# Optimization experiments

Measured on AMD Instinct MI355X. Metric: run time of the kernel, lower is better.

## Reference

```python
import jax, jax.numpy as jnp
import numpy as np

EPS = 1e-5  # pyg LayerNorm default eps


def _graph_ln(x):
    # pyg.nn.norm.LayerNorm(affine=False), default mode='graph', batch=None:
    # normalizes over ALL elements of the tensor (x - x.mean()) / x.std(unbiased=False)
    m = x.mean()
    v = jnp.mean((x - m) ** 2)
    return (x - m) * jax.lax.rsqrt(v + EPS)


def _cheb_conv(x, row, col, w, W, b):
    # ChebConv, normalization='sym', lambda_max=2 => scaled Laplacian
    # L_hat = L - I = -D^{-1/2} A D^{-1/2} (self-loops removed, weighted)
    # x: [B,N,C_in], row/col: [E], w: [E], W: [K,C_in,C_out], b: [C_out]
    N = x.shape[1]
    w = jnp.where(row == col, 0.0, w)  # remove_self_loops
    deg = jnp.zeros((N,), x.dtype).at[row].add(w)
    dinv = jnp.where(deg > 0, jax.lax.rsqrt(jnp.maximum(deg, 1e-12)), 0.0)
    norm = -(dinv[row] * w * dinv[col])  # [E]

    def prop(t):  # out[i] += norm_e * t[j] for edge (j=row -> i=col)
        msg = norm[None, :, None] * t[:, row, :]  # [B,E,C]
        return jnp.zeros_like(t).at[:, col, :].add(msg)

    Tx0 = x
    out = jnp.einsum('bnc,cd->bnd', Tx0, W[0])
    Tx1 = prop(x)
    out = out + jnp.einsum('bnc,cd->bnd', Tx1, W[1])
    for k in range(2, W.shape[0]):
        Tx2 = 2.0 * prop(Tx1) - Tx0
        out = out + jnp.einsum('bnc,cd->bnd', Tx2, W[k])
        Tx0, Tx1 = Tx1, Tx2
    return out + b


def setup_inputs() -> dict:
    key = jax.random.key(0)
    ks = jax.random.split(key, 8)
    B, N, C, E, L, K = 8, 2048, 256, 32768, 3, 3
    node_feature = jax.random.normal(ks[0], (B, N, C), dtype=jnp.float32)
    edge_index = jax.random.randint(ks[1], (L, 2, E), 0, N)
    edge_weight = jax.random.uniform(ks[2], (L, E), dtype=jnp.float32)
    s = 1.0 / np.sqrt(C)
    cheb_w = jax.random.normal(ks[3], (L, K, C, C), dtype=jnp.float32) * s
    cheb_b = jnp.zeros((L, C), dtype=jnp.float32)
    mlp_w = jax.random.normal(ks[4], (L, C, C), dtype=jnp.float32) * s
    mlp_b = jax.random.normal(ks[5], (L, C), dtype=jnp.float32) * 0.01
    return {"node_feature": node_feature, "edge_weight": edge_weight,
            "cheb_w": cheb_w, "cheb_b": cheb_b, "mlp_w": mlp_w,
            "mlp_b": mlp_b, "edge_index": edge_index}


def reference(node_feature, edge_weight, cheb_w, cheb_b, mlp_w, mlp_b, edge_index):
    h = node_feature  # [B,N,C]
    L = cheb_w.shape[0]
    for l in range(L):
        h_res = h
        hn = _graph_ln(h)
        hc = _cheb_conv(hn, edge_index[l, 0], edge_index[l, 1],
                        edge_weight[l], cheb_w[l], cheb_b[l])
        h = hc + h_res
        h_res = h
        hn = _graph_ln(h)
        hm = jax.nn.gelu(jnp.einsum('bnc,cd->bnd', hn, mlp_w[l]) + mlp_b[l],
                         approximate=False)  # dropout is identity at inference
        h = hm + h_res
    return h.mean(axis=1)  # [B,C]
```

## Files before the change

kernel.cpp:

```cpp
#include <hip/hip_runtime.h>

#define BATCH   8
#define NNODE   2048
#define CH      256
#define NEDGE   32768
#define NLAYER  3
#define MROWS   (NNODE*BATCH)
#define KCAT    (3*CH)
#define NTOT    (MROWS*CH)

typedef _Float16 half8 __attribute__((ext_vector_type(8)));
typedef _Float16 half4 __attribute__((ext_vector_type(4)));
typedef float    f32x4 __attribute__((ext_vector_type(4)));

#define OFF_ACAT   ((size_t)0)
#define OFF_HF     ((size_t)25165824)
#define OFF_WT     ((size_t)33554432)
#define OFF_MT     ((size_t)34734080)
#define OFF_PARTA  ((size_t)35127296)
#define OFF_PARTB  ((size_t)35135488)
#define OFF_CS     ((size_t)35143680)
#define OFF_CSM    ((size_t)35152896)
#define OFF_DEG    ((size_t)35155968)
#define OFF_CNT    ((size_t)35180544)
#define OFF_ELIST  ((size_t)35205120)
#define OFF_R1     ((size_t)36777984)
#define OFF_R2     ((size_t)36802560)

__device__ __forceinline__ void async_lds16(const void* g, void* l) {
  __builtin_amdgcn_global_load_lds((const __attribute__((address_space(1))) void*)g,
                                   (__attribute__((address_space(3))) void*)l, 16, 0, 0);
}

__global__ __launch_bounds__(256) void k_init(const float* __restrict__ x,
                                              _Float16* __restrict__ Acat,
                                              float2* __restrict__ part,
                                              const float* __restrict__ cheb_w,
                                              const float* __restrict__ mlp_w,
                                              _Float16* __restrict__ Wt,
                                              _Float16* __restrict__ Mt,
                                              float* __restrict__ deg,
                                              unsigned int* __restrict__ count) {
  __shared__ float rs[512];
  __shared__ _Float16 lt[64][72];
  const int blk = blockIdx.x, t = threadIdx.x;
  if (blk < 1024) {
    int tid = blk*256 + t;
    float s = 0.f, s2 = 0.f;
    for (int i = tid; i < NTOT/4; i += 1024*256) {
      int c4 = i & 63, b = (i >> 6) & 7, n = i >> 9;
      float4 v = ((const float4*)x)[((b*NNODE + n) << 6) + c4];
      half4 o; o[0]=(_Float16)v.x; o[1]=(_Float16)v.y; o[2]=(_Float16)v.z; o[3]=(_Float16)v.w;
      *(half4*)&Acat[(size_t)(i >> 6)*KCAT + c4*4] = o;
      s  += v.x + v.y + v.z + v.w;
      s2 += v.x*v.x + v.y*v.y + v.z*v.z + v.w*v.w;
    }
    rs[t] = s; rs[256+t] = s2; __syncthreads();
    for (int o = 128; o > 0; o >>= 1) {
      if (t < o) { rs[t] += rs[t+o]; rs[256+t] += rs[256+t+o]; }
      __syncthreads();
    }
    if (t == 0) part[blk] = make_float2(rs[0], rs[256]);
  } else if (blk < 1048) {
    int i = (blk - 1024)*256 + t;
    if (i < NLAYER*NNODE) { deg[i] = 0.f; count[i] = 0u; }
  } else {
    const int tile = blk - 1048;
    const int rr = t >> 4, c4 = t & 15;
    if (tile < 144) {
      const int l = tile / 48, rem = tile % 48;
      const int kk = rem / 16, q = rem % 16, ci = q >> 2, ni = q & 3;
      const float4* W  = (const float4*)cheb_w + ((size_t)((l*3 + kk)*CH + ci*64))*64 + ni*16;
      const float4* W2 = (const float4*)cheb_w + ((size_t)((l*3 + 2 )*CH + ci*64))*64 + ni*16;
      #pragma unroll
      for (int p = 0; p < 4; ++p) {
        const int r = p*16 + rr;
        float4 v = W[(size_t)r*64 + c4];
        if (kk == 0) {
          float4 v2 = W2[(size_t)r*64 + c4];
          v.x -= v2.x; v.y -= v2.y; v.z -= v2.z; v.w -= v2.w;
        } else if (kk == 2) {
          v.x *= 2.f; v.y *= 2.f; v.z *= 2.f; v.w *= 2.f;
        }
        lt[c4*4+0][r] = (_Float16)v.x; lt[c4*4+1][r] = (_Float16)v.y;
        lt[c4*4+2][r] = (_Float16)v.z; lt[c4*4+3][r] = (_Float16)v.w;
      }
      __syncthreads();
      const int nr = t >> 2, ch2 = t & 3;
      #pragma unroll
      for (int pp = 0; pp < 2; ++pp) {
        const int ch = ch2 + pp*4;
        half8 v = *(const half8*)&lt[nr][ch*8];
        *(half8*)&Wt[((size_t)(l*CH + ni*64 + nr))*KCAT + kk*256 + ci*64 + ch*8] = v;
      }
    } else {
      const int m = tile - 144;
      const int l = m / 16, q = m % 16, ci = q >> 2, ni = q & 3;
      const float4* W = (const float4*)mlp_w + ((size_t)(l*CH + ci*64))*64 + ni*16;
      #pragma unroll
      for (int p = 0; p < 4; ++p) {
        const int r = p*16 + rr;
        float4 v = W[(size_t)r*64 + c4];
        lt[c4*4+0][r] = (_Float16)v.x; lt[c4*4+1][r] = (_Float16)v.y;
        lt[c4*4+2][r] = (_Float16)v.z; lt[c4*4+3][r] = (_Float16)v.w;
      }
      __syncthreads();
      const int nr = t >> 2, ch2 = t & 3;
      #pragma unroll
      for (int pp = 0; pp < 2; ++pp) {
        const int ch = ch2 + pp*4;
        half8 v = *(const half8*)&lt[nr][ch*8];
        *(half8*)&Mt[((size_t)(l*CH + ni*64 + nr))*CH + ci*64 + ch*8] = v;
      }
    }
  }
}

__global__ __launch_bounds__(256) void k_edge_scatter(const int* __restrict__ ei,
                                                      const float* __restrict__ ew,
                                                      float* deg, unsigned int* count,
                                                      unsigned int* elist,
                                                      const _Float16* __restrict__ Wt,
                                                      const _Float16* __restrict__ Mt,
                                                      float* __restrict__ cs,
                                                      float* __restrict__ csM,
                                                      float* __restrict__ out_zero) {
  const int blk = blockIdx.x, t = threadIdx.x;
  if (blk < 384) {
    int i = blk*256 + t;
    int l = i / NEDGE, e = i % NEDGE;
    const int* rows = ei + l*2*NEDGE;
    const int* cols = rows + NEDGE;
    int r = rows[e], c = cols[e];
    float w = (r == c) ? 0.f : ew[i];
    atomicAdd(&deg[l*NNODE + r], w);
    unsigned int slot = atomicAdd(&count[l*NNODE + c], 1u);
    if (slot < 64u) elist[(size_t)(l*NNODE + c)*64 + slot] = (unsigned int)e;
  } else if (blk < 393) {
    int idx = blk - 384, l = idx / 3, kk = idx % 3, n = t;
    const half8* row = (const half8*)&Wt[((size_t)(l*CH + n))*KCAT + kk*256];
    float s = 0.f;
    #pragma unroll 4
    for (int j = 0; j < 32; ++j) {
      half8 v = row[j];
      s += (float)v[0]+(float)v[1]+(float)v[2]+(float)v[3]
         + (float)v[4]+(float)v[5]+(float)v[6]+(float)v[7];
    }
    cs[(l*3 + kk)*CH + n] = s;
  } else if (blk < 396) {
    int l = blk - 393, n = t;
    const half8* row = (const half8*)&Mt[((size_t)(l*CH + n))*CH];
    float s = 0.f;
    #pragma unroll 4
    for (int j = 0; j < 32; ++j) {
      half8 v = row[j];
      s += (float)v[0]+(float)v[1]+(float)v[2]+(float)v[3]
         + (float)v[4]+(float)v[5]+(float)v[6]+(float)v[7];
    }
    csM[l*CH + n] = s;
  } else {
    for (int i = t; i < BATCH*CH; i += 256) out_zero[i] = 0.f;
  }
}

template<int SRC_OFF, int DST_OFF, int RMODE>
__global__ __launch_bounds__(256) void k_prop(_Float16* __restrict__ Acat,
                                              const int* __restrict__ rows,
                                              const float* __restrict__ ew_l,
                                              const float* __restrict__ deg_l,
                                              const unsigned int* __restrict__ count,
                                              const unsigned int* __restrict__ el,
                                              float* __restrict__ r1_l,
                                              float* __restrict__ r2_l) {
  const int blk = blockIdx.x, t = threadIdx.x;
  const int b = blk & 7, dgrp = blk >> 3;
  const int w = t >> 6, lane = t & 63;
  const int dst = dgrp*4 + w;
  unsigned int c = count[dst]; if (c > 64u) c = 64u;
  const float dc = deg_l[dst];
  const float ic = dc > 0.f ? rsqrtf(fmaxf(dc, 1e-12f)) : 0.f;
  int srcv = 0; float nmv = 0.f;
  if (lane < (int)c) {
    unsigned int e = el[(size_t)dst*64 + lane];
    srcv = rows[e];
    float wv = (srcv == dst) ? 0.f : ew_l[e];
    float dr = deg_l[srcv];
    float ir = dr > 0.f ? rsqrtf(fmaxf(dr, 1e-12f)) : 0.f;
    nmv = -(ir * wv * ic);
  }
  if (RMODE && b == 0) {
    float rv = nmv;
    if (RMODE == 2) rv = (lane < (int)c) ? nmv * r1_l[srcv] : 0.f;
    #pragma unroll
    for (int o = 32; o > 0; o >>= 1) rv += __shfl_xor(rv, o);
    if (lane == 0) { if (RMODE == 1) r1_l[dst] = rv; else r2_l[dst] = rv; }
  }
  float a0 = 0.f, a1 = 0.f, a2 = 0.f, a3 = 0.f;
  const _Float16* base = Acat + SRC_OFF + b*KCAT + lane*4;
  #define PROP_STEP(i)                                                            \
    {                                                                             \
      int   src = __builtin_amdgcn_readlane(srcv, (i));                           \
      int   nbi = __builtin_amdgcn_readlane(__builtin_bit_cast(int, nmv), (i));   \
      float nm  = __builtin_bit_cast(float, nbi);                                 \
      half4 v = *(const half4*)&base[(size_t)src*8*KCAT];                         \
      a0 += nm*(float)v[0]; a1 += nm*(float)v[1];                                 \
      a2 += nm*(float)v[2]; a3 += nm*(float)v[3];                                 \
    }
  unsigned int i = 0;
  for (; i + 4 <= c; i += 4) { PROP_STEP(i) PROP_STEP(i+1) PROP_STEP(i+2) PROP_STEP(i+3) }
  for (; i < c; ++i) { PROP_STEP(i) }
  #undef PROP_STEP
  half4 o; o[0] = (_Float16)a0; o[1] = (_Float16)a1; o[2] = (_Float16)a2; o[3] = (_Float16)a3;
  *(half4*)&Acat[(size_t)(dst*8 + b)*KCAT + DST_OFF + lane*4] = o;
}

template<int KSTEPS, int DO_GELU>
__global__ __launch_bounds__(256) void k_gemm(const _Float16* __restrict__ A, int lda,
                                              const _Float16* __restrict__ Bt, int ldb,
                                              const float* __restrict__ bias,
                                              const float* __restrict__ cs,
                                              const float* __restrict__ r1,
                                              const float* __restrict__ r2,
                                              const float2* __restrict__ part_in,
                                              float2* __restrict__ part_out,
                                              const _Float16* __restrict__ R, int ldr,
                                              _Float16* __restrict__ O, int ldo) {
  __shared__ _Float16 Als[64*64];
  __shared__ _Float16 Bls[64*64];
  __shared__ float red[512];
  __shared__ float mv[2];
  const int bm = blockIdx.x, bn = blockIdx.y;
  const int t = threadIdx.x;
  const int w = t >> 6, lane = t & 63;
  const int quad = lane >> 4, l16 = lane & 15;
  const int wm = w & 1, wn = w >> 1;

  {
    float s = 0.f, s2 = 0.f;
    for (int i = t; i < 1024; i += 256) { float2 p = part_in[i]; s += p.x; s2 += p.y; }
    red[t] = s; red[256+t] = s2; __syncthreads();
    for (int o = 128; o > 0; o >>= 1) {
      if (t < o) { red[t] += red[t+o]; red[256+t] += red[256+t+o]; }
      __syncthreads();
    }
    if (t == 0) {
      float mean = red[0] * (1.f/(float)NTOT);
      float var  = red[256] * (1.f/(float)NTOT) - mean*mean;
      mv[0] = mean; mv[1] = rsqrtf(var + 1e-5f);
    }
    __syncthreads();
  }
  const float mean = mv[0], istd = mv[1];

  f32x4 acc00 = {0.f,0.f,0.f,0.f};
  f32x4 acc01 = acc00, acc10 = acc00, acc11 = acc00;

  const int c0 = w*64 + lane, c1 = 256 + w*64 + lane;
  const int r0 = c0 >> 3, s0 = (c0 & 7) ^ (r0 & 7);
  const int r1i = c1 >> 3, s1 = (c1 & 7) ^ (r1i & 7);
  const _Float16* ga0 = A  + (size_t)(bm*64 + r0)*lda + s0*8;
  const _Float16* ga1 = A  + (size_t)(bm*64 + r1i)*lda + s1*8;
  const _Float16* gb0 = Bt + (size_t)(bn*64 + r0)*ldb + s0*8;
  const _Float16* gb1 = Bt + (size_t)(bn*64 + r1i)*ldb + s1*8;
  _Float16* lA0 = &Als[w*512];
  _Float16* lA1 = &Als[2048 + w*512];
  _Float16* lB0 = &Bls[w*512];
  _Float16* lB1 = &Bls[2048 + w*512];

  const int ra0 = wm*32 + l16, ra1 = ra0 + 16;
  const int rb0 = wn*32 + l16, rb1 = rb0 + 16;

  for (int ks = 0; ks < KSTEPS; ++ks) {
    async_lds16(ga0, lA0); async_lds16(ga1, lA1);
    async_lds16(gb0, lB0); async_lds16(gb1, lB1);
    ga0 += 64; ga1 += 64; gb0 += 64; gb1 += 64;
    __syncthreads();
    #pragma unroll
    for (int kh = 0; kh < 2; ++kh) {
      const int q = kh*4 + quad;
      half8 a0 = *(const half8*)&Als[ra0*64 + (q ^ (ra0 & 7))*8];
      half8 a1 = *(const half8*)&Als[ra1*64 + (q ^ (ra1 & 7))*8];
      half8 b0 = *(const half8*)&Bls[rb0*64 + (q ^ (rb0 & 7))*8];
      half8 b1 = *(const half8*)&Bls[rb1*64 + (q ^ (rb1 & 7))*8];
      acc00 = __builtin_amdgcn_mfma_f32_16x16x32_f16(a0, b0, acc00, 0, 0, 0);
      acc01 = __builtin_amdgcn_mfma_f32_16x16x32_f16(a0, b1, acc01, 0, 0, 0);
      acc10 = __builtin_amdgcn_mfma_f32_16x16x32_f16(a1, b0, acc10, 0, 0, 0);
      acc11 = __builtin_amdgcn_mfma_f32_16x16x32_f16(a1, b1, acc11, 0, 0, 0);
    }
    __syncthreads();
  }

  float s = 0.f, s2 = 0.f;
  const int gm0 = bm*64 + wm*32, gn0 = bn*64 + wn*32;
  const float mi = -mean * istd;
  #pragma unroll
  for (int i = 0; i < 2; ++i) {
    #pragma unroll
    for (int j = 0; j < 2; ++j) {
      f32x4 a = (i == 0) ? (j == 0 ? acc00 : acc01) : (j == 0 ? acc10 : acc11);
      const int col = gn0 + j*16 + l16;
      const float bv = bias[col];
      const float c0v = cs[col];
      float c1v = 0.f, c2v = 0.f;
      if (!DO_GELU) { c1v = cs[256 + col]; c2v = cs[512 + col]; }
      #pragma unroll
      for (int r = 0; r < 4; ++r) {
        const int row = gm0 + i*16 + quad*4 + r;
        float v;
        if (DO_GELU) {
          v = istd*a[r] + mi*c0v + bv;
          v = 0.5f*v*(1.f + erff(v*0.70710678118654752f));
        } else {
          const int node = row >> 3;
          v = istd*a[r] + mi*(c0v + r1[node]*c1v + r2[node]*c2v) + bv;
        }
        float hv = (float)R[(size_t)row*ldr + col] + v;
        O[(size_t)row*ldo + col] = (_Float16)hv;
        s += hv; s2 += hv*hv;
      }
    }
  }
  red[t] = s; red[256+t] = s2; __syncthreads();
  for (int o = 128; o > 0; o >>= 1) {
    if (t < o) { red[t] += red[t+o]; red[256+t] += red[256+t+o]; }
    __syncthreads();
  }
  if (t == 0) part_out[blockIdx.y*gridDim.x + blockIdx.x] = make_float2(red[0], red[256]);
}

__global__ __launch_bounds__(256) void k_mean(const _Float16* __restrict__ Acat,
                                              float* __restrict__ out) {
  int b = blockIdx.x & 7, chunk = blockIdx.x >> 3;
  int c = threadIdx.x;
  float s = 0.f;
  for (int k = 0; k < 256; ++k) {
    int n = chunk*256 + k;
    s += (float)Acat[(size_t)(n*8 + b)*KCAT + c];
  }
  atomicAdd(&out[(b << 8) + c], s * (1.f/(float)NNODE));
}

extern "C" void kernel_launch(void* const* d_in, const int* in_sizes, int n_in,
                              void* d_out, int out_size, void* d_ws, size_t ws_size,
                              hipStream_t stream) {
  const float* x      = (const float*)d_in[0];
  const float* ew     = (const float*)d_in[1];
  const float* cheb_w = (const float*)d_in[2];
  const float* cheb_b = (const float*)d_in[3];
  const float* mlp_w  = (const float*)d_in[4];
  const float* mlp_b  = (const float*)d_in[5];
  const int*   ei     = (const int*)d_in[6];
  float* out = (float*)d_out;

  char* ws = (char*)d_ws;
  _Float16*     Acat  = (_Float16*)(ws + OFF_ACAT);
  _Float16*     Hf    = (_Float16*)(ws + OFF_HF);
  _Float16*     Wt    = (_Float16*)(ws + OFF_WT);
  _Float16*     Mt    = (_Float16*)(ws + OFF_MT);
  float2*       partA = (float2*)(ws + OFF_PARTA);
  float2*       partB = (float2*)(ws + OFF_PARTB);
  float*        cs    = (float*)(ws + OFF_CS);
  float*        csM   = (float*)(ws + OFF_CSM);
  float*        deg   = (float*)(ws + OFF_DEG);
  unsigned int* cnt   = (unsigned int*)(ws + OFF_CNT);
  unsigned int* elist = (unsigned int*)(ws + OFF_ELIST);
  float*        r1    = (float*)(ws + OFF_R1);
  float*        r2    = (float*)(ws + OFF_R2);

  k_init<<<1240, 256, 0, stream>>>(x, Acat, partA, cheb_w, mlp_w, Wt, Mt, deg, cnt);
  k_edge_scatter<<<397, 256, 0, stream>>>(ei, ew, deg, cnt, elist, Wt, Mt, cs, csM, out);

  for (int l = 0; l < NLAYER; ++l) {
    const int* rows_l = ei + l*2*NEDGE;
    const float* ew_l = ew + l*NEDGE;
    const float* deg_l = deg + l*NNODE;
    const unsigned int* cnt_l = cnt + l*NNODE;
    const unsigned int* el_l  = elist + (size_t)l*NNODE*64;
    float* r1_l = r1 + l*NNODE;
    float* r2_l = r2 + l*NNODE;

    k_prop<0, 256, 1><<<4096, 256, 0, stream>>>(
        Acat, rows_l, ew_l, deg_l, cnt_l, el_l, r1_l, r2_l);
    k_prop<256, 512, 2><<<4096, 256, 0, stream>>>(
        Acat, rows_l, ew_l, deg_l, cnt_l, el_l, r1_l, r2_l);
    k_gemm<12, 0><<<dim3(256, 4), 256, 0, stream>>>(
        Acat, KCAT, Wt + (size_t)l*CH*KCAT, KCAT, cheb_b + l*CH,
        cs + l*3*CH, r1_l, r2_l, partA, partB,
        Acat, KCAT, Hf, CH);
    k_gemm<4, 1><<<dim3(256, 4), 256, 0, stream>>>(
        Hf, CH, Mt + (size_t)l*CH*CH, CH, mlp_b + l*CH,
        csM + l*CH, r1_l, r2_l, partB, partA,
        Hf, CH, Acat, KCAT);
  }

  k_mean<<<64, 256, 0, stream>>>(Acat, out);
}
```

Before: 287.6 us.

## Enlarge GEMM tile to 128x64, widen prop loads, halve partial-sum blocks

The GEMM kernels now compute a 128x64 output tile per block, with each wave holding 4x2 MFMA accumulators. This doubles A-tile LDS and the register footprint but reuses B fragments across more rows, and it halves the grid. The propagation kernel now has each wave cover two batches with 8-wide half loads per lane, halving its block count and widening the gather accesses. The init kernel's statistics partials are cut from 1024 to 512 blocks, and the GEMM reducers read only NPART entries.

Result: faster. 274.8 us (-4.5%).

```diff
diff --git a/kernel.cpp b/kernel.cpp
--- a/kernel.cpp
+++ b/kernel.cpp
@@ -27,6 +27,8 @@
 #define OFF_R1     ((size_t)36777984)
 #define OFF_R2     ((size_t)36802560)
 
+#define NPART 512
+
 __device__ __forceinline__ void async_lds16(const void* g, void* l) {
   __builtin_amdgcn_global_load_lds((const __attribute__((address_space(1))) void*)g,
                                    (__attribute__((address_space(3))) void*)l, 16, 0, 0);
@@ -44,10 +46,10 @@
   __shared__ float rs[512];
   __shared__ _Float16 lt[64][72];
   const int blk = blockIdx.x, t = threadIdx.x;
-  if (blk < 1024) {
+  if (blk < 512) {
     int tid = blk*256 + t;
     float s = 0.f, s2 = 0.f;
-    for (int i = tid; i < NTOT/4; i += 1024*256) {
+    for (int i = tid; i < NTOT/4; i += 512*256) {
       int c4 = i & 63, b = (i >> 6) & 7, n = i >> 9;
       float4 v = ((const float4*)x)[((b*NNODE + n) << 6) + c4];
       half4 o; o[0]=(_Float16)v.x; o[1]=(_Float16)v.y; o[2]=(_Float16)v.z; o[3]=(_Float16)v.w;
@@ -61,11 +63,11 @@
       __syncthreads();
     }
     if (t == 0) part[blk] = make_float2(rs[0], rs[256]);
-  } else if (blk < 1048) {
-    int i = (blk - 1024)*256 + t;
+  } else if (blk < 536) {
+    int i = (blk - 512)*256 + t;
     if (i < NLAYER*NNODE) { deg[i] = 0.f; count[i] = 0u; }
   } else {
-    const int tile = blk - 1048;
+    const int tile = blk - 536;
     const int rr = t >> 4, c4 = t & 15;
     if (tile < 144) {
       const int l = tile / 48, rem = tile % 48;
@@ -173,9 +175,10 @@
                                               float* __restrict__ r1_l,
                                               float* __restrict__ r2_l) {
   const int blk = blockIdx.x, t = threadIdx.x;
-  const int b = blk & 7, dgrp = blk >> 3;
+  const int bp = blk & 3, dgrp = blk >> 2;
   const int w = t >> 6, lane = t & 63;
   const int dst = dgrp*4 + w;
+  const int b = bp*2 + (lane >> 5), l32 = lane & 31;
   unsigned int c = count[dst]; if (c > 64u) c = 64u;
   const float dc = deg_l[dst];
   const float ic = dc > 0.f ? rsqrtf(fmaxf(dc, 1e-12f)) : 0.f;
@@ -188,30 +191,34 @@
     float ir = dr > 0.f ? rsqrtf(fmaxf(dr, 1e-12f)) : 0.f;
     nmv = -(ir * wv * ic);
   }
-  if (RMODE && b == 0) {
+  if (RMODE && bp == 0) {
     float rv = nmv;
     if (RMODE == 2) rv = (lane < (int)c) ? nmv * r1_l[srcv] : 0.f;
     #pragma unroll
     for (int o = 32; o > 0; o >>= 1) rv += __shfl_xor(rv, o);
     if (lane == 0) { if (RMODE == 1) r1_l[dst] = rv; else r2_l[dst] = rv; }
   }
-  float a0 = 0.f, a1 = 0.f, a2 = 0.f, a3 = 0.f;
-  const _Float16* base = Acat + SRC_OFF + b*KCAT + lane*4;
+  float a0=0.f,a1=0.f,a2=0.f,a3=0.f,a4=0.f,a5=0.f,a6=0.f,a7=0.f;
+  const _Float16* base = Acat + SRC_OFF + (size_t)b*KCAT + l32*8;
   #define PROP_STEP(i)                                                            \
     {                                                                             \
       int   src = __builtin_amdgcn_readlane(srcv, (i));                           \
       int   nbi = __builtin_amdgcn_readlane(__builtin_bit_cast(int, nmv), (i));   \
       float nm  = __builtin_bit_cast(float, nbi);                                 \
-      half4 v = *(const half4*)&base[(size_t)src*8*KCAT];                         \
+      half8 v = *(const half8*)&base[(size_t)src*8*KCAT];                         \
       a0 += nm*(float)v[0]; a1 += nm*(float)v[1];                                 \
       a2 += nm*(float)v[2]; a3 += nm*(float)v[3];                                 \
+      a4 += nm*(float)v[4]; a5 += nm*(float)v[5];                                 \
+      a6 += nm*(float)v[6]; a7 += nm*(float)v[7];                                 \
     }
   unsigned int i = 0;
   for (; i + 4 <= c; i += 4) { PROP_STEP(i) PROP_STEP(i+1) PROP_STEP(i+2) PROP_STEP(i+3) }
   for (; i < c; ++i) { PROP_STEP(i) }
   #undef PROP_STEP
-  half4 o; o[0] = (_Float16)a0; o[1] = (_Float16)a1; o[2] = (_Float16)a2; o[3] = (_Float16)a3;
-  *(half4*)&Acat[(size_t)(dst*8 + b)*KCAT + DST_OFF + lane*4] = o;
+  half8 o;
+  o[0]=(_Float16)a0; o[1]=(_Float16)a1; o[2]=(_Float16)a2; o[3]=(_Float16)a3;
+  o[4]=(_Float16)a4; o[5]=(_Float16)a5; o[6]=(_Float16)a6; o[7]=(_Float16)a7;
+  *(half8*)&Acat[(size_t)(dst*8 + b)*KCAT + DST_OFF + l32*8] = o;
 }
 
 template<int KSTEPS, int DO_GELU>
@@ -225,7 +232,7 @@
                                               float2* __restrict__ part_out,
                                               const _Float16* __restrict__ R, int ldr,
                                               _Float16* __restrict__ O, int ldo) {
-  __shared__ _Float16 Als[64*64];
+  __shared__ _Float16 Als[128*64];
   __shared__ _Float16 Bls[64*64];
   __shared__ float red[512];
   __shared__ float mv[2];
@@ -233,11 +240,11 @@
   const int t = threadIdx.x;
   const int w = t >> 6, lane = t & 63;
   const int quad = lane >> 4, l16 = lane & 15;
-  const int wm = w & 1, wn = w >> 1;
+  const int rw = w & 1, cw = w >> 1;
 
   {
     float s = 0.f, s2 = 0.f;
-    for (int i = t; i < 1024; i += 256) { float2 p = part_in[i]; s += p.x; s2 += p.y; }
+    for (int i = t; i < NPART; i += 256) { float2 p = part_in[i]; s += p.x; s2 += p.y; }
     red[t] = s; red[256+t] = s2; __syncthreads();
     for (int o = 128; o > 0; o >>= 1) {
       if (t < o) { red[t] += red[t+o]; red[256+t] += red[256+t+o]; }
@@ -252,52 +259,64 @@
   }
   const float mean = mv[0], istd = mv[1];
 
-  f32x4 acc00 = {0.f,0.f,0.f,0.f};
-  f32x4 acc01 = acc00, acc10 = acc00, acc11 = acc00;
-
-  const int c0 = w*64 + lane, c1 = 256 + w*64 + lane;
-  const int r0 = c0 >> 3, s0 = (c0 & 7) ^ (r0 & 7);
-  const int r1i = c1 >> 3, s1 = (c1 & 7) ^ (r1i & 7);
-  const _Float16* ga0 = A  + (size_t)(bm*64 + r0)*lda + s0*8;
-  const _Float16* ga1 = A  + (size_t)(bm*64 + r1i)*lda + s1*8;
-  const _Float16* gb0 = Bt + (size_t)(bn*64 + r0)*ldb + s0*8;
-  const _Float16* gb1 = Bt + (size_t)(bn*64 + r1i)*ldb + s1*8;
+  f32x4 acc[4][2];
+  #pragma unroll
+  for (int i = 0; i < 4; ++i)
+    #pragma unroll
+    for (int j = 0; j < 2; ++j) acc[i][j] = (f32x4){0.f,0.f,0.f,0.f};
+
+  const int cA0 = t, cA1 = 256+t, cA2 = 512+t, cA3 = 768+t;
+  const int rA0 = cA0>>3, sA0 = (cA0&7)^(rA0&7);
+  const int rA1 = cA1>>3, sA1 = (cA1&7)^(rA1&7);
+  const int rA2 = cA2>>3, sA2 = (cA2&7)^(rA2&7);
+  const int rA3 = cA3>>3, sA3 = (cA3&7)^(rA3&7);
+  const _Float16* ga0 = A + (size_t)(bm*128 + rA0)*lda + sA0*8;
+  const _Float16* ga1 = A + (size_t)(bm*128 + rA1)*lda + sA1*8;
+  const _Float16* ga2 = A + (size_t)(bm*128 + rA2)*lda + sA2*8;
+  const _Float16* ga3 = A + (size_t)(bm*128 + rA3)*lda + sA3*8;
+  const _Float16* gb0 = Bt + (size_t)(bn*64 + rA0)*ldb + sA0*8;
+  const _Float16* gb1 = Bt + (size_t)(bn*64 + rA1)*ldb + sA1*8;
   _Float16* lA0 = &Als[w*512];
   _Float16* lA1 = &Als[2048 + w*512];
+  _Float16* lA2 = &Als[4096 + w*512];
+  _Float16* lA3 = &Als[6144 + w*512];
   _Float16* lB0 = &Bls[w*512];
   _Float16* lB1 = &Bls[2048 + w*512];
 
-  const int ra0 = wm*32 + l16, ra1 = ra0 + 16;
-  const int rb0 = wn*32 + l16, rb1 = rb0 + 16;
-
   for (int ks = 0; ks < KSTEPS; ++ks) {
     async_lds16(ga0, lA0); async_lds16(ga1, lA1);
+    async_lds16(ga2, lA2); async_lds16(ga3, lA3);
     async_lds16(gb0, lB0); async_lds16(gb1, lB1);
-    ga0 += 64; ga1 += 64; gb0 += 64; gb1 += 64;
+    ga0 += 64; ga1 += 64; ga2 += 64; ga3 += 64; gb0 += 64; gb1 += 64;
     __syncthreads();
     #pragma unroll
     for (int kh = 0; kh < 2; ++kh) {
       const int q = kh*4 + quad;
-      half8 a0 = *(const half8*)&Als[ra0*64 + (q ^ (ra0 & 7))*8];
-      half8 a1 = *(const half8*)&Als[ra1*64 + (q ^ (ra1 & 7))*8];
-      half8 b0 = *(const half8*)&Bls[rb0*64 + (q ^ (rb0 & 7))*8];
-      half8 b1 = *(const half8*)&Bls[rb1*64 + (q ^ (rb1 & 7))*8];
-      acc00 = __builtin_amdgcn_mfma_f32_16x16x32_f16(a0, b0, acc00, 0, 0, 0);
-      acc01 = __builtin_amdgcn_mfma_f32_16x16x32_f16(a0, b1, acc01, 0, 0, 0);
-      acc10 = __builtin_amdgcn_mfma_f32_16x16x32_f16(a1, b0, acc10, 0, 0, 0);
-      acc11 = __builtin_amdgcn_mfma_f32_16x16x32_f16(a1, b1, acc11, 0, 0, 0);
+      half8 bf[2];
+      #pragma unroll
+      for (int j = 0; j < 2; ++j) {
+        const int rb = cw*32 + j*16 + l16;
+        bf[j] = *(const half8*)&Bls[rb*64 + (q ^ (rb & 7))*8];
+      }
+      #pragma unroll
+      for (int i = 0; i < 4; ++i) {
+        const int ra = rw*64 + i*16 + l16;
+        half8 af = *(const half8*)&Als[ra*64 + (q ^ (ra & 7))*8];
+        acc[i][0] = __builtin_amdgcn_mfma_f32_16x16x32_f16(af, bf[0], acc[i][0], 0, 0, 0);
+        acc[i][1] = __builtin_amdgcn_mfma_f32_16x16x32_f16(af, bf[1], acc[i][1], 0, 0, 0);
+      }
     }
     __syncthreads();
   }
 
   float s = 0.f, s2 = 0.f;
-  const int gm0 = bm*64 + wm*32, gn0 = bn*64 + wn*32;
+  const int gm0 = bm*128 + rw*64, gn0 = bn*64 + cw*32;
   const float mi = -mean * istd;
   #pragma unroll
-  for (int i = 0; i < 2; ++i) {
+  for (int i = 0; i < 4; ++i) {
     #pragma unroll
     for (int j = 0; j < 2; ++j) {
-      f32x4 a = (i == 0) ? (j == 0 ? acc00 : acc01) : (j == 0 ? acc10 : acc11);
+      f32x4 a = acc[i][j];
       const int col = gn0 + j*16 + l16;
       const float bv = bias[col];
       const float c0v = cs[col];
@@ -367,7 +386,7 @@
   float*        r1    = (float*)(ws + OFF_R1);
   float*        r2    = (float*)(ws + OFF_R2);
 
-  k_init<<<1240, 256, 0, stream>>>(x, Acat, partA, cheb_w, mlp_w, Wt, Mt, deg, cnt);
+  k_init<<<728, 256, 0, stream>>>(x, Acat, partA, cheb_w, mlp_w, Wt, Mt, deg, cnt);
   k_edge_scatter<<<397, 256, 0, stream>>>(ei, ew, deg, cnt, elist, Wt, Mt, cs, csM, out);
 
   for (int l = 0; l < NLAYER; ++l) {
@@ -379,15 +398,15 @@
     float* r1_l = r1 + l*NNODE;
     float* r2_l = r2 + l*NNODE;
 
-    k_prop<0, 256, 1><<<4096, 256, 0, stream>>>(
+    k_prop<0, 256, 1><<<2048, 256, 0, stream>>>(
         Acat, rows_l, ew_l, deg_l, cnt_l, el_l, r1_l, r2_l);
-    k_prop<256, 512, 2><<<4096, 256, 0, stream>>>(
+    k_prop<256, 512, 2><<<2048, 256, 0, stream>>>(
         Acat, rows_l, ew_l, deg_l, cnt_l, el_l, r1_l, r2_l);
-    k_gemm<12, 0><<<dim3(256, 4), 256, 0, stream>>>(
+    k_gemm<12, 0><<<dim3(128, 4), 256, 0, stream>>>(
         Acat, KCAT, Wt + (size_t)l*CH*KCAT, KCAT, cheb_b + l*CH,
         cs + l*3*CH, r1_l, r2_l, partA, partB,
         Acat, KCAT, Hf, CH);
-    k_gemm<4, 1><<<dim3(256, 4), 256, 0, stream>>>(
+    k_gemm<4, 1><<<dim3(128, 4), 256, 0, stream>>>(
         Hf, CH, Mt + (size_t)l*CH*CH, CH, mlp_b + l*CH,
         csM + l*CH, r1_l, r2_l, partB, partA,
         Hf, CH, Acat, KCAT);
```
